# Kernel optimization log

Measured on AMD Instinct MI355X. Metric: run time of the kernel, lower is better.

Reference implementation:

```python
import jax, jax.numpy as jnp
import numpy as np

TEMP = 1.0  # temperature

def setup_inputs() -> dict:
    key = jax.random.key(0)
    ks = jax.random.split(key, 16)
    B, Cin, Cout, H, W, K, kk, A = 32, 64, 64, 128, 128, 4, 3, 16
    c_ = Cin + Cout
    r = lambda k, s: jax.random.normal(k, s, dtype=jnp.float32)
    return {
        'x': r(ks[0], (B, Cin, H, W)),
        'fc_w': r(ks[1], (A, Cin)) * 0.1,
        'ch_w': r(ks[2], (Cin, A)) * 0.1,
        'ch_b': jnp.zeros((Cin,), jnp.float32),
        'f_w': r(ks[3], (Cout, A)) * 0.1,
        'f_b': jnp.zeros((Cout,), jnp.float32),
        'sp_w': r(ks[4], (kk * kk, A)) * 0.1,
        'sp_b': jnp.zeros((kk * kk,), jnp.float32),
        'k_w': r(ks[5], (K, A)) * 0.1,
        'k_b': jnp.zeros((K,), jnp.float32),
        'fus_w1': r(ks[6], (c_ // 16, c_)) * 0.1,
        'fus_b1': jnp.zeros((c_ // 16,), jnp.float32),
        'fus_w2': r(ks[7], (c_, c_ // 16)) * 0.1,
        'fus_b2': jnp.zeros((c_,), jnp.float32),
        'weight': r(ks[8], (K, Cout, Cin, kk, kk)) * (1.0 / np.sqrt(Cin * kk * kk)),
    }

def reference(x, fc_w, ch_w, ch_b, f_w, f_b, sp_w, sp_b, k_w, k_b,
              fus_w1, fus_b1, fus_w2, fus_b2, weight):
    B, Cin, H, W = x.shape
    K, Cout, _, kk, _ = weight.shape
    # --- Attention branches (on globally pooled features) ---
    pooled = x.mean(axis=(2, 3))                      # (B, Cin)
    a = jax.nn.relu(pooled @ fc_w.T)                  # (B, A)
    ch_att = jax.nn.sigmoid(a @ ch_w.T + ch_b)        # (B, Cin)
    f_att = jax.nn.sigmoid(a @ f_w.T + f_b)           # (B, Cout)
    sp_att = jax.nn.sigmoid(a @ sp_w.T + sp_b).reshape(B, 1, 1, 1, kk, kk)
    k_att = jax.nn.softmax((a @ k_w.T + k_b) / TEMP, axis=1).reshape(B, K, 1, 1, 1, 1)
    # --- Attention fusion ---
    att = jnp.concatenate([ch_att, f_att], axis=1)    # (B, Cin+Cout)
    att2 = jax.nn.sigmoid(jax.nn.relu(att @ fus_w1.T + fus_b1) @ fus_w2.T + fus_b2)
    s1 = att2[:, :Cin].sum(axis=1)
    s2 = att2[:, Cin:].sum(axis=1)
    score = jax.nn.softmax(jnp.stack([s1, s2], axis=1) / TEMP, axis=1)
    w1 = score[:, 0][:, None, None, None]
    w2 = score[:, 1][:, None, None, None]
    # --- Apply channel attention, aggregate per-sample weights ---
    xm = w1 * x * ch_att[:, :, None, None]
    # (B,K,1,1,kk,kk)*(B,K,1,1,1,1)*(1,K,Cout,Cin,kk,kk) summed over K
    agg_w = (sp_att * k_att * weight[None]).sum(axis=1)  # (B, Cout, Cin, kk, kk)
    # --- Per-sample conv2d (stride 1, padding 1) ---
    def conv_one(xb, wb):
        return jax.lax.conv_general_dilated(
            xb[None], wb, window_strides=(1, 1), padding=[(1, 1), (1, 1)],
            dimension_numbers=('NCHW', 'OIHW', 'NCHW'))[0]
    out = jax.vmap(conv_one)(xm, agg_w)               # (B, Cout, H, W)
    return w2 * out * f_att[:, :, None, None]
```

## Files before the change

### kernel.cpp

```cpp
#include <hip/hip_runtime.h>
#include <math.h>
#include <stdint.h>

typedef short bf16x8 __attribute__((ext_vector_type(8)));
typedef float f32x16 __attribute__((ext_vector_type(16)));

#define WS_POOLED 0
#define WS_CIN    2048
#define WS_COUT   4096
#define WS_SP9    6144
#define WS_K4     6432
#define WS_WF     8192

static __device__ __forceinline__ unsigned f2bf(float f) {
  unsigned u = __builtin_bit_cast(unsigned, f);
  return (u + 0x7FFFu + ((u >> 16) & 1u)) >> 16;
}

__global__ __launch_bounds__(256) void pool_kernel(const float* __restrict__ x,
                                                   float* __restrict__ pooled) {
  const int bc = blockIdx.x;
  const int tid = threadIdx.x;
  const float4* p = (const float4*)(x + (size_t)bc * 16384);
  float s = 0.f;
  for (int j = tid; j < 4096; j += 256) {
    float4 v = p[j];
    s += (v.x + v.y) + (v.z + v.w);
  }
#pragma unroll
  for (int off = 32; off > 0; off >>= 1) s += __shfl_down(s, off, 64);
  __shared__ float red[4];
  if ((tid & 63) == 0) red[tid >> 6] = s;
  __syncthreads();
  if (tid == 0) pooled[bc] = (red[0] + red[1] + red[2] + red[3]) * (1.f / 16384.f);
}

__global__ __launch_bounds__(128) void att_kernel(
    const float* __restrict__ fc_w, const float* __restrict__ ch_w, const float* __restrict__ ch_b,
    const float* __restrict__ f_w,  const float* __restrict__ f_b,
    const float* __restrict__ sp_w, const float* __restrict__ sp_b,
    const float* __restrict__ k_w,  const float* __restrict__ k_b,
    const float* __restrict__ fus_w1, const float* __restrict__ fus_b1,
    const float* __restrict__ fus_w2, const float* __restrict__ fus_b2,
    float* __restrict__ ws) {
  const int b = blockIdx.x;
  const int t = threadIdx.x;
  __shared__ float s_pool[64], s_a[16], s_att[128], s_sp[9], s_k[4], s_h[8],
      s_att2[128], s_red[2], s_w12[2];

  if (t < 64) s_pool[t] = ws[WS_POOLED + b * 64 + t];
  __syncthreads();

  if (t < 16) {
    float s = 0.f;
    for (int c = 0; c < 64; ++c) s += s_pool[c] * fc_w[t * 64 + c];
    s_a[t] = fmaxf(s, 0.f);
  }
  __syncthreads();

  if (t < 64) {
    float s = ch_b[t];
    for (int j = 0; j < 16; ++j) s += s_a[j] * ch_w[t * 16 + j];
    s_att[t] = 1.f / (1.f + expf(-s));
  } else {
    const int o = t - 64;
    float s = f_b[o];
    for (int j = 0; j < 16; ++j) s += s_a[j] * f_w[o * 16 + j];
    s_att[t] = 1.f / (1.f + expf(-s));
  }
  if (t < 9) {
    float s = sp_b[t];
    for (int j = 0; j < 16; ++j) s += s_a[j] * sp_w[t * 16 + j];
    s_sp[t] = 1.f / (1.f + expf(-s));
  }
  if (t < 4) {
    float s = k_b[t];
    for (int j = 0; j < 16; ++j) s += s_a[j] * k_w[t * 16 + j];
    s_k[t] = s;
  }
  __syncthreads();

  if (t < 8) {
    float s = fus_b1[t];
    for (int c = 0; c < 128; ++c) s += s_att[c] * fus_w1[t * 128 + c];
    s_h[t] = fmaxf(s, 0.f);
  }
  if (t == 127) {
    float m = fmaxf(fmaxf(s_k[0], s_k[1]), fmaxf(s_k[2], s_k[3]));
    float e0 = expf(s_k[0] - m), e1 = expf(s_k[1] - m);
    float e2 = expf(s_k[2] - m), e3 = expf(s_k[3] - m);
    float inv = 1.f / (e0 + e1 + e2 + e3);
    s_k[0] = e0 * inv; s_k[1] = e1 * inv; s_k[2] = e2 * inv; s_k[3] = e3 * inv;
  }
  __syncthreads();

  {
    float s = fus_b2[t];
    for (int j = 0; j < 8; ++j) s += s_h[j] * fus_w2[t * 8 + j];
    s_att2[t] = 1.f / (1.f + expf(-s));
  }
  __syncthreads();

  if (t < 2) {
    float s = 0.f;
    for (int c = 0; c < 64; ++c) s += s_att2[t * 64 + c];
    s_red[t] = s;
  }
  __syncthreads();
  if (t == 0) {
    float m = fmaxf(s_red[0], s_red[1]);
    float e1 = expf(s_red[0] - m), e2 = expf(s_red[1] - m);
    float inv = 1.f / (e1 + e2);
    s_w12[0] = e1 * inv;
    s_w12[1] = e2 * inv;
  }
  __syncthreads();

  if (t < 64) {
    ws[WS_CIN  + b * 64 + t] = s_w12[0] * s_att[t];
    ws[WS_COUT + b * 64 + t] = s_w12[1] * s_att[64 + t];
  }
  if (t < 9) ws[WS_SP9 + b * 9 + t] = s_sp[t];
  if (t < 4) ws[WS_K4 + b * 4 + t] = s_k[t];
}

__global__ __launch_bounds__(256) void wf_kernel(const float* __restrict__ weight,
                                                 const float* __restrict__ ws,
                                                 unsigned short* __restrict__ wfb) {
  const int bo = blockIdx.x;
  const int b = bo >> 6, o = bo & 63;
  const float co = ws[WS_COUT + b * 64 + o];
  const float k0 = ws[WS_K4 + b * 4 + 0], k1 = ws[WS_K4 + b * 4 + 1];
  const float k2 = ws[WS_K4 + b * 4 + 2], k3 = ws[WS_K4 + b * 4 + 3];
  for (int idx = threadIdx.x; idx < 576; idx += 256) {
    const int pq = idx >> 6, i = idx & 63;
    const size_t wi = ((size_t)o * 64 + i) * 9 + pq;
    float s = k0 * weight[wi] + k1 * weight[36864 + wi] +
              k2 * weight[73728 + wi] + k3 * weight[110592 + wi];
    float v = co * ws[WS_SP9 + b * 9 + pq] * ws[WS_CIN + b * 64 + i] * s;
    wfb[((size_t)(b * 9 + pq) * 64 + o) * 64 + i] = (unsigned short)f2bf(v);
  }
}

__global__ __launch_bounds__(512, 2) void conv_kernel(const float* __restrict__ x,
                                                      const unsigned short* __restrict__ wfb,
                                                      float* __restrict__ out) {
  const int b  = blockIdx.x >> 5;
  const int h0 = (blockIdx.x & 31) << 2;
  const int tid = threadIdx.x;
  const int lane = tid & 63;
  const int wid = tid >> 6;
  const int rw = wid >> 1;
  const int obase = (wid & 1) << 5;
  const int l31 = lane & 31;
  const int hi = lane >> 5;

  __shared__ __align__(16) short sx[6 * 132 * 16];
  __shared__ __align__(16) short swf[576 * 16];

  f32x16 acc[4];
#pragma unroll
  for (int nt = 0; nt < 4; ++nt)
#pragma unroll
    for (int r = 0; r < 16; ++r) acc[nt][r] = 0.f;

  for (int ch = 0; ch < 4; ++ch) {
    const int c0 = ch << 4;
    __syncthreads();
    for (int idx = tid; idx < 1584; idx += 512) {
      const int c = idx % 132;
      const int t = idx / 132;
      const int r = t % 6;
      const int h8 = t / 6;
      const int gr = h0 - 1 + r, gc = c - 1;
      uint4 v = make_uint4(0u, 0u, 0u, 0u);
      if ((unsigned)gr < 128u && (unsigned)gc < 128u) {
        const float* xp = x + (((size_t)(b * 64 + c0 + h8 * 8) * 128 + gr) * 128 + gc);
        v.x = f2bf(xp[0])          | (f2bf(xp[16384])     << 16);
        v.y = f2bf(xp[2 * 16384])  | (f2bf(xp[3 * 16384]) << 16);
        v.z = f2bf(xp[4 * 16384])  | (f2bf(xp[5 * 16384]) << 16);
        v.w = f2bf(xp[6 * 16384])  | (f2bf(xp[7 * 16384]) << 16);
      }
      const int pix = r * 132 + c;
      const int byteoff = (pix * 32 + h8 * 16) ^ ((pix & 4) << 2);
      *(uint4*)((char*)sx + byteoff) = v;
    }
    for (int idx = tid; idx < 1152; idx += 512) {
      const int row = idx >> 1, h8 = idx & 1;
      uint4 v = *(const uint4*)(wfb + (((size_t)b * 576 + row) * 64 + c0 + h8 * 8));
      const int byteoff = (row * 32 + h8 * 16) ^ ((row & 4) << 2);
      *(uint4*)((char*)swf + byteoff) = v;
    }
    __syncthreads();

#pragma unroll
    for (int p = 0; p < 3; ++p) {
#pragma unroll
      for (int q = 0; q < 3; ++q) {
        const int arow = (p * 3 + q) * 64 + obase + l31;
        const int abyte = (arow * 32 + hi * 16) ^ ((arow & 4) << 2);
        bf16x8 af = *(const bf16x8*)((const char*)swf + abyte);
#pragma unroll
        for (int nt = 0; nt < 4; ++nt) {
          const int pix = (rw + p) * 132 + nt * 32 + q + l31;
          const int bbyte = (pix * 32 + hi * 16) ^ ((pix & 4) << 2);
          bf16x8 bf = *(const bf16x8*)((const char*)sx + bbyte);
          acc[nt] = __builtin_amdgcn_mfma_f32_32x32x16_bf16(af, bf, acc[nt], 0, 0, 0);
        }
      }
    }
  }

  const int h = h0 + rw;
#pragma unroll
  for (int nt = 0; nt < 4; ++nt) {
    const int col = nt * 32 + l31;
#pragma unroll
    for (int reg = 0; reg < 16; ++reg) {
      const int o = obase + (reg & 3) + ((reg >> 2) << 3) + (hi << 2);
      out[(((size_t)(b * 64 + o)) * 128 + h) * 128 + col] = acc[nt][reg];
    }
  }
}

extern "C" void kernel_launch(void* const* d_in, const int* in_sizes, int n_in,
                              void* d_out, int out_size, void* d_ws, size_t ws_size,
                              hipStream_t stream) {
  const float* x      = (const float*)d_in[0];
  const float* fc_w   = (const float*)d_in[1];
  const float* ch_w   = (const float*)d_in[2];
  const float* ch_b   = (const float*)d_in[3];
  const float* f_w    = (const float*)d_in[4];
  const float* f_b    = (const float*)d_in[5];
  const float* sp_w   = (const float*)d_in[6];
  const float* sp_b   = (const float*)d_in[7];
  const float* k_w    = (const float*)d_in[8];
  const float* k_b    = (const float*)d_in[9];
  const float* fus_w1 = (const float*)d_in[10];
  const float* fus_b1 = (const float*)d_in[11];
  const float* fus_w2 = (const float*)d_in[12];
  const float* fus_b2 = (const float*)d_in[13];
  const float* weight = (const float*)d_in[14];
  float* ws  = (float*)d_ws;
  float* out = (float*)d_out;
  unsigned short* wfb = (unsigned short*)(ws + WS_WF);

  pool_kernel<<<2048, 256, 0, stream>>>(x, ws + WS_POOLED);
  att_kernel<<<32, 128, 0, stream>>>(fc_w, ch_w, ch_b, f_w, f_b, sp_w, sp_b,
                                     k_w, k_b, fus_w1, fus_b1, fus_w2, fus_b2, ws);
  wf_kernel<<<2048, 256, 0, stream>>>(weight, ws, wfb);
  conv_kernel<<<1024, 512, 0, stream>>>(x, wfb, out);
}
```

Before: 137.3 us.

## Fuse pooling with bf16 NHWC conversion of x and feed conv from bf16

Adds a convert kernel that reads x once, writes a channel-last bf16 copy and per-block partial sums for pooling. This replaces the separate pool pass. The conv kernel then loads bf16 channel-contiguous tiles straight into shared memory, with lower register use so four blocks can share a CU, instead of converting fp32 NCHW inside the conv. It needs a workspace of about 67 MB and falls back to the old path when the workspace is smaller; the bf16 write and re-read add traffic of their own.

```diff
diff --git a/kernel.cpp b/kernel.cpp
--- a/kernel.cpp
+++ b/kernel.cpp
@@ -4,6 +4,7 @@
 
 typedef short bf16x8 __attribute__((ext_vector_type(8)));
 typedef float f32x16 __attribute__((ext_vector_type(16)));
+typedef unsigned short ushort_t;
 
 #define WS_POOLED 0
 #define WS_CIN    2048
@@ -12,9 +13,57 @@
 #define WS_K4     6432
 #define WS_WF     8192
 
+#define NP_CIN  65536
+#define NP_COUT 67584
+#define NP_SP9  69632
+#define NP_K4   69920
+#define NP_WFB_BYTES (512 * 1024)
+#define NP_XB_BYTES  (3 * 1024 * 1024)
+#define NP_NEED ((size_t)(3 * 1024 * 1024) + (size_t)(64 * 1024 * 1024))
+
 static __device__ __forceinline__ unsigned f2bf(float f) {
   unsigned u = __builtin_bit_cast(unsigned, f);
   return (u + 0x7FFFu + ((u >> 16) & 1u)) >> 16;
+}
+
+__global__ __launch_bounds__(256) void convert_kernel(const float* __restrict__ x,
+                                                      ushort_t* __restrict__ xb,
+                                                      float* __restrict__ part) {
+  const int b = blockIdx.x >> 5;
+  const int g = blockIdx.x & 31;
+  const int p0 = g << 9;
+  const int t = threadIdx.x;
+  const int w = t >> 6;
+  const int lane = t & 63;
+  __shared__ float s_part[4 * 64];
+
+  const int pa = p0 + 2 * t;
+  ushort_t* outp = xb + (size_t)(b * 16384 + pa) * 64;
+
+#pragma unroll 1
+  for (int g8 = 0; g8 < 8; ++g8) {
+    uint4 ca, cb;
+    unsigned* cap = (unsigned*)&ca;
+    unsigned* cbp = (unsigned*)&cb;
+#pragma unroll
+    for (int j = 0; j < 8; ++j) {
+      const int ci = g8 * 8 + j;
+      float2 v = *(const float2*)(x + ((size_t)(b * 64 + ci) * 16384) + pa);
+      float psum = v.x + v.y;
+#pragma unroll
+      for (int off = 32; off > 0; off >>= 1) psum += __shfl_down(psum, off, 64);
+      if (lane == 0) s_part[w * 64 + ci] = psum;
+      unsigned ba = f2bf(v.x), bb = f2bf(v.y);
+      if (j & 1) { cap[j >> 1] |= ba << 16; cbp[j >> 1] |= bb << 16; }
+      else       { cap[j >> 1]  = ba;       cbp[j >> 1]  = bb; }
+    }
+    *(uint4*)(outp + g8 * 8)      = ca;
+    *(uint4*)(outp + 64 + g8 * 8) = cb;
+  }
+  __syncthreads();
+  if (t < 64)
+    part[((size_t)b * 32 + g) * 64 + t] =
+        s_part[t] + s_part[64 + t] + s_part[128 + t] + s_part[192 + t];
 }
 
 __global__ __launch_bounds__(256) void pool_kernel(const float* __restrict__ x,
@@ -36,19 +85,29 @@
 }
 
 __global__ __launch_bounds__(128) void att_kernel(
+    const float* __restrict__ pin, int n_part,
     const float* __restrict__ fc_w, const float* __restrict__ ch_w, const float* __restrict__ ch_b,
     const float* __restrict__ f_w,  const float* __restrict__ f_b,
     const float* __restrict__ sp_w, const float* __restrict__ sp_b,
     const float* __restrict__ k_w,  const float* __restrict__ k_b,
     const float* __restrict__ fus_w1, const float* __restrict__ fus_b1,
     const float* __restrict__ fus_w2, const float* __restrict__ fus_b2,
-    float* __restrict__ ws) {
+    float* __restrict__ o_cin, float* __restrict__ o_cout,
+    float* __restrict__ o_sp9, float* __restrict__ o_k4) {
   const int b = blockIdx.x;
   const int t = threadIdx.x;
   __shared__ float s_pool[64], s_a[16], s_att[128], s_sp[9], s_k[4], s_h[8],
       s_att2[128], s_red[2], s_w12[2];
 
-  if (t < 64) s_pool[t] = ws[WS_POOLED + b * 64 + t];
+  if (t < 64) {
+    if (n_part > 0) {
+      float s = 0.f;
+      for (int g = 0; g < n_part; ++g) s += pin[((size_t)b * n_part + g) * 64 + t];
+      s_pool[t] = s * (1.f / 16384.f);
+    } else {
+      s_pool[t] = pin[b * 64 + t];
+    }
+  }
   __syncthreads();
 
   if (t < 16) {
@@ -117,34 +176,106 @@
   __syncthreads();
 
   if (t < 64) {
-    ws[WS_CIN  + b * 64 + t] = s_w12[0] * s_att[t];
-    ws[WS_COUT + b * 64 + t] = s_w12[1] * s_att[64 + t];
-  }
-  if (t < 9) ws[WS_SP9 + b * 9 + t] = s_sp[t];
-  if (t < 4) ws[WS_K4 + b * 4 + t] = s_k[t];
+    o_cin[b * 64 + t]  = s_w12[0] * s_att[t];
+    o_cout[b * 64 + t] = s_w12[1] * s_att[64 + t];
+  }
+  if (t < 9) o_sp9[b * 9 + t] = s_sp[t];
+  if (t < 4) o_k4[b * 4 + t] = s_k[t];
 }
 
 __global__ __launch_bounds__(256) void wf_kernel(const float* __restrict__ weight,
-                                                 const float* __restrict__ ws,
-                                                 unsigned short* __restrict__ wfb) {
+                                                 const float* __restrict__ cin,
+                                                 const float* __restrict__ cout_,
+                                                 const float* __restrict__ sp9,
+                                                 const float* __restrict__ k4,
+                                                 ushort_t* __restrict__ wfb) {
   const int bo = blockIdx.x;
   const int b = bo >> 6, o = bo & 63;
-  const float co = ws[WS_COUT + b * 64 + o];
-  const float k0 = ws[WS_K4 + b * 4 + 0], k1 = ws[WS_K4 + b * 4 + 1];
-  const float k2 = ws[WS_K4 + b * 4 + 2], k3 = ws[WS_K4 + b * 4 + 3];
+  const float co = cout_[b * 64 + o];
+  const float k0 = k4[b * 4 + 0], k1 = k4[b * 4 + 1];
+  const float k2 = k4[b * 4 + 2], k3 = k4[b * 4 + 3];
   for (int idx = threadIdx.x; idx < 576; idx += 256) {
     const int pq = idx >> 6, i = idx & 63;
     const size_t wi = ((size_t)o * 64 + i) * 9 + pq;
     float s = k0 * weight[wi] + k1 * weight[36864 + wi] +
               k2 * weight[73728 + wi] + k3 * weight[110592 + wi];
-    float v = co * ws[WS_SP9 + b * 9 + pq] * ws[WS_CIN + b * 64 + i] * s;
-    wfb[((size_t)(b * 9 + pq) * 64 + o) * 64 + i] = (unsigned short)f2bf(v);
-  }
-}
-
-__global__ __launch_bounds__(512, 2) void conv_kernel(const float* __restrict__ x,
-                                                      const unsigned short* __restrict__ wfb,
-                                                      float* __restrict__ out) {
+    float v = co * sp9[b * 9 + pq] * cin[b * 64 + i] * s;
+    wfb[((size_t)(b * 9 + pq) * 64 + o) * 64 + i] = (ushort_t)f2bf(v);
+  }
+}
+
+__global__ __launch_bounds__(512, 4) void conv_bf16(const ushort_t* __restrict__ xb,
+                                                    const ushort_t* __restrict__ wfb,
+                                                    float* __restrict__ out) {
+  const int b  = blockIdx.x >> 5;
+  const int h0 = (blockIdx.x & 31) << 2;
+  const int tid = threadIdx.x;
+  const int lane = tid & 63;
+  const int wid = tid >> 6;
+  const int rw = wid >> 1;
+  const int obase = (wid & 1) << 5;
+  const int l31 = lane & 31;
+  const int hi = lane >> 5;
+
+  __shared__ __align__(16) short sx[792 * 16];
+
+  f32x16 acc[4];
+#pragma unroll
+  for (int nt = 0; nt < 4; ++nt)
+#pragma unroll
+    for (int r = 0; r < 16; ++r) acc[nt][r] = 0.f;
+
+  const ushort_t* wfb_b = wfb + (size_t)b * 9 * 64 * 64;
+  const ushort_t* xb_b  = xb + (size_t)b * 16384 * 64;
+
+  for (int ch = 0; ch < 4; ++ch) {
+    const int c0 = ch << 4;
+    __syncthreads();
+    for (int s = tid; s < 1584; s += 512) {
+      const int pix = s >> 1, hseg = s & 1;
+      const int r = pix / 132;
+      const int c = pix - r * 132;
+      const int gr = h0 - 1 + r, gc = c - 1;
+      uint4 v = make_uint4(0u, 0u, 0u, 0u);
+      if ((unsigned)gr < 128u && (unsigned)gc < 128u)
+        v = *(const uint4*)(xb_b + (size_t)(gr * 128 + gc) * 64 + c0 + hseg * 8);
+      *(uint4*)((char*)sx + s * 16) = v;
+    }
+    bf16x8 af[9];
+#pragma unroll
+    for (int tap = 0; tap < 9; ++tap)
+      af[tap] = *(const bf16x8*)(wfb_b + ((tap * 64 + obase + l31) * 64) + c0 + hi * 8);
+    __syncthreads();
+
+#pragma unroll
+    for (int p = 0; p < 3; ++p) {
+#pragma unroll
+      for (int q = 0; q < 3; ++q) {
+#pragma unroll
+        for (int nt = 0; nt < 4; ++nt) {
+          const int pix = (rw + p) * 132 + nt * 32 + q + l31;
+          bf16x8 bf = *(const bf16x8*)((const char*)sx + pix * 32 + hi * 16);
+          acc[nt] = __builtin_amdgcn_mfma_f32_32x32x16_bf16(af[p * 3 + q], bf, acc[nt], 0, 0, 0);
+        }
+      }
+    }
+  }
+
+  const int h = h0 + rw;
+#pragma unroll
+  for (int nt = 0; nt < 4; ++nt) {
+    const int col = nt * 32 + l31;
+#pragma unroll
+    for (int reg = 0; reg < 16; ++reg) {
+      const int o = obase + (reg & 3) + ((reg >> 2) << 3) + (hi << 2);
+      out[(((size_t)(b * 64 + o)) * 128 + h) * 128 + col] = acc[nt][reg];
+    }
+  }
+}
+
+__global__ __launch_bounds__(512, 2) void conv_fp32(const float* __restrict__ x,
+                                                    const ushort_t* __restrict__ wfb,
+                                                    float* __restrict__ out) {
   const int b  = blockIdx.x >> 5;
   const int h0 = (blockIdx.x & 31) << 2;
   const int tid = threadIdx.x;
@@ -243,11 +374,31 @@
   const float* weight = (const float*)d_in[14];
   float* ws  = (float*)d_ws;
   float* out = (float*)d_out;
-  unsigned short* wfb = (unsigned short*)(ws + WS_WF);
-
-  pool_kernel<<<2048, 256, 0, stream>>>(x, ws + WS_POOLED);
-  att_kernel<<<32, 128, 0, stream>>>(fc_w, ch_w, ch_b, f_w, f_b, sp_w, sp_b,
-                                     k_w, k_b, fus_w1, fus_b1, fus_w2, fus_b2, ws);
-  wf_kernel<<<2048, 256, 0, stream>>>(weight, ws, wfb);
-  conv_kernel<<<1024, 512, 0, stream>>>(x, wfb, out);
-}
+
+  if (ws_size >= NP_NEED) {
+    float* part  = ws;
+    float* cin   = ws + NP_CIN;
+    float* cout_ = ws + NP_COUT;
+    float* sp9   = ws + NP_SP9;
+    float* k4    = ws + NP_K4;
+    ushort_t* wfb = (ushort_t*)((char*)d_ws + NP_WFB_BYTES);
+    ushort_t* xb  = (ushort_t*)((char*)d_ws + NP_XB_BYTES);
+
+    convert_kernel<<<1024, 256, 0, stream>>>(x, xb, part);
+    att_kernel<<<32, 128, 0, stream>>>(part, 32, fc_w, ch_w, ch_b, f_w, f_b,
+                                       sp_w, sp_b, k_w, k_b, fus_w1, fus_b1,
+                                       fus_w2, fus_b2, cin, cout_, sp9, k4);
+    wf_kernel<<<2048, 256, 0, stream>>>(weight, cin, cout_, sp9, k4, wfb);
+    conv_bf16<<<1024, 512, 0, stream>>>(xb, wfb, out);
+  } else {
+    ushort_t* wfb = (ushort_t*)(ws + WS_WF);
+    pool_kernel<<<2048, 256, 0, stream>>>(x, ws + WS_POOLED);
+    att_kernel<<<32, 128, 0, stream>>>(ws + WS_POOLED, 0, fc_w, ch_w, ch_b, f_w, f_b,
+                                       sp_w, sp_b, k_w, k_b, fus_w1, fus_b1,
+                                       fus_w2, fus_b2, ws + WS_CIN, ws + WS_COUT,
+                                       ws + WS_SP9, ws + WS_K4);
+    wf_kernel<<<2048, 256, 0, stream>>>(weight, ws + WS_CIN, ws + WS_COUT,
+                                        ws + WS_SP9, ws + WS_K4, wfb);
+    conv_fp32<<<1024, 512, 0, stream>>>(x, wfb, out);
+  }
+}
```

Result: slower. 277.4 us (+102.0%).

## Vectorize conv input staging, read weights from global, raise occupancy

Applied to the files above, without the earlier changes.

The conv kernel now stages the input tile with float4 loads: each of 408 threads loads 4 consecutive pixels across 8 channels, converts them to bf16 and writes them into a wider 136-column padded, XOR-swizzled LDS tile. The weight tile is no longer staged in LDS. MFMA A-fragments are read straight from global memory, which roughly halves LDS use and lets launch bounds rise to 4 blocks per CU. The aim is to cut scalar strided global loads and LDS traffic and to raise occupancy. The cost is repeated global/L2 reads of weights inside the MFMA loop and possible register pressure under the tighter bound. The attention and weight-fusion kernels are only refactored to take separate pointers.

```diff
diff --git a/kernel.cpp b/kernel.cpp
--- a/kernel.cpp
+++ b/kernel.cpp
@@ -4,6 +4,7 @@
 
 typedef short bf16x8 __attribute__((ext_vector_type(8)));
 typedef float f32x16 __attribute__((ext_vector_type(16)));
+typedef unsigned short ushort_t;
 
 #define WS_POOLED 0
 #define WS_CIN    2048
@@ -36,19 +37,21 @@
 }
 
 __global__ __launch_bounds__(128) void att_kernel(
+    const float* __restrict__ pooled,
     const float* __restrict__ fc_w, const float* __restrict__ ch_w, const float* __restrict__ ch_b,
     const float* __restrict__ f_w,  const float* __restrict__ f_b,
     const float* __restrict__ sp_w, const float* __restrict__ sp_b,
     const float* __restrict__ k_w,  const float* __restrict__ k_b,
     const float* __restrict__ fus_w1, const float* __restrict__ fus_b1,
     const float* __restrict__ fus_w2, const float* __restrict__ fus_b2,
-    float* __restrict__ ws) {
+    float* __restrict__ o_cin, float* __restrict__ o_cout,
+    float* __restrict__ o_sp9, float* __restrict__ o_k4) {
   const int b = blockIdx.x;
   const int t = threadIdx.x;
   __shared__ float s_pool[64], s_a[16], s_att[128], s_sp[9], s_k[4], s_h[8],
       s_att2[128], s_red[2], s_w12[2];
 
-  if (t < 64) s_pool[t] = ws[WS_POOLED + b * 64 + t];
+  if (t < 64) s_pool[t] = pooled[b * 64 + t];
   __syncthreads();
 
   if (t < 16) {
@@ -117,33 +120,36 @@
   __syncthreads();
 
   if (t < 64) {
-    ws[WS_CIN  + b * 64 + t] = s_w12[0] * s_att[t];
-    ws[WS_COUT + b * 64 + t] = s_w12[1] * s_att[64 + t];
-  }
-  if (t < 9) ws[WS_SP9 + b * 9 + t] = s_sp[t];
-  if (t < 4) ws[WS_K4 + b * 4 + t] = s_k[t];
+    o_cin[b * 64 + t]  = s_w12[0] * s_att[t];
+    o_cout[b * 64 + t] = s_w12[1] * s_att[64 + t];
+  }
+  if (t < 9) o_sp9[b * 9 + t] = s_sp[t];
+  if (t < 4) o_k4[b * 4 + t] = s_k[t];
 }
 
 __global__ __launch_bounds__(256) void wf_kernel(const float* __restrict__ weight,
-                                                 const float* __restrict__ ws,
-                                                 unsigned short* __restrict__ wfb) {
+                                                 const float* __restrict__ cin,
+                                                 const float* __restrict__ cout_,
+                                                 const float* __restrict__ sp9,
+                                                 const float* __restrict__ k4,
+                                                 ushort_t* __restrict__ wfb) {
   const int bo = blockIdx.x;
   const int b = bo >> 6, o = bo & 63;
-  const float co = ws[WS_COUT + b * 64 + o];
-  const float k0 = ws[WS_K4 + b * 4 + 0], k1 = ws[WS_K4 + b * 4 + 1];
-  const float k2 = ws[WS_K4 + b * 4 + 2], k3 = ws[WS_K4 + b * 4 + 3];
+  const float co = cout_[b * 64 + o];
+  const float k0 = k4[b * 4 + 0], k1 = k4[b * 4 + 1];
+  const float k2 = k4[b * 4 + 2], k3 = k4[b * 4 + 3];
   for (int idx = threadIdx.x; idx < 576; idx += 256) {
     const int pq = idx >> 6, i = idx & 63;
     const size_t wi = ((size_t)o * 64 + i) * 9 + pq;
     float s = k0 * weight[wi] + k1 * weight[36864 + wi] +
               k2 * weight[73728 + wi] + k3 * weight[110592 + wi];
-    float v = co * ws[WS_SP9 + b * 9 + pq] * ws[WS_CIN + b * 64 + i] * s;
-    wfb[((size_t)(b * 9 + pq) * 64 + o) * 64 + i] = (unsigned short)f2bf(v);
-  }
-}
-
-__global__ __launch_bounds__(512, 2) void conv_kernel(const float* __restrict__ x,
-                                                      const unsigned short* __restrict__ wfb,
+    float v = co * sp9[b * 9 + pq] * cin[b * 64 + i] * s;
+    wfb[((size_t)(b * 9 + pq) * 64 + o) * 64 + i] = (ushort_t)f2bf(v);
+  }
+}
+
+__global__ __launch_bounds__(512, 4) void conv_kernel(const float* __restrict__ x,
+                                                      const ushort_t* __restrict__ wfb,
                                                       float* __restrict__ out) {
   const int b  = blockIdx.x >> 5;
   const int h0 = (blockIdx.x & 31) << 2;
@@ -155,8 +161,7 @@
   const int l31 = lane & 31;
   const int hi = lane >> 5;
 
-  __shared__ __align__(16) short sx[6 * 132 * 16];
-  __shared__ __align__(16) short swf[576 * 16];
+  __shared__ __align__(16) short sx[816 * 16];
 
   f32x16 acc[4];
 #pragma unroll
@@ -164,32 +169,40 @@
 #pragma unroll
     for (int r = 0; r < 16; ++r) acc[nt][r] = 0.f;
 
+  const ushort_t* wfb_b = wfb + (size_t)b * 9 * 64 * 64;
+
+  const bool sactive = tid < 408;
+  int so = 0, sr = 0, sc = 0;
+  if (sactive) { so = tid / 204; const int rem = tid % 204; sr = rem / 34; sc = rem % 34; }
+  const int gr  = h0 - 1 + sr;
+  const int gcb = sc * 4 - 4;
+  const bool inb = sactive && ((unsigned)gr < 128u) && ((unsigned)gcb < 128u);
+  const int pixb = sr * 136 + sc * 4;
+  const int key = ((pixb >> 2) & 7) << 4;
+  const float* xrow = x + ((size_t)(b * 64) * 16384) + gr * 128 + gcb;
+
   for (int ch = 0; ch < 4; ++ch) {
-    const int c0 = ch << 4;
     __syncthreads();
-    for (int idx = tid; idx < 1584; idx += 512) {
-      const int c = idx % 132;
-      const int t = idx / 132;
-      const int r = t % 6;
-      const int h8 = t / 6;
-      const int gr = h0 - 1 + r, gc = c - 1;
-      uint4 v = make_uint4(0u, 0u, 0u, 0u);
-      if ((unsigned)gr < 128u && (unsigned)gc < 128u) {
-        const float* xp = x + (((size_t)(b * 64 + c0 + h8 * 8) * 128 + gr) * 128 + gc);
-        v.x = f2bf(xp[0])          | (f2bf(xp[16384])     << 16);
-        v.y = f2bf(xp[2 * 16384])  | (f2bf(xp[3 * 16384]) << 16);
-        v.z = f2bf(xp[4 * 16384])  | (f2bf(xp[5 * 16384]) << 16);
-        v.w = f2bf(xp[6 * 16384])  | (f2bf(xp[7 * 16384]) << 16);
+    if (inb) {
+      const int c0 = ch * 16 + so * 8;
+      float4 v[8];
+#pragma unroll
+      for (int j = 0; j < 8; ++j)
+        v[j] = *(const float4*)(xrow + (size_t)(c0 + j) * 16384);
+#pragma unroll
+      for (int j = 0; j < 4; ++j) {
+        uint4 u;
+        u.x = f2bf(((const float*)&v[0])[j]) | (f2bf(((const float*)&v[1])[j]) << 16);
+        u.y = f2bf(((const float*)&v[2])[j]) | (f2bf(((const float*)&v[3])[j]) << 16);
+        u.z = f2bf(((const float*)&v[4])[j]) | (f2bf(((const float*)&v[5])[j]) << 16);
+        u.w = f2bf(((const float*)&v[6])[j]) | (f2bf(((const float*)&v[7])[j]) << 16);
+        *(uint4*)((char*)sx + ((((pixb + j) * 32) + so * 16) ^ key)) = u;
       }
-      const int pix = r * 132 + c;
-      const int byteoff = (pix * 32 + h8 * 16) ^ ((pix & 4) << 2);
-      *(uint4*)((char*)sx + byteoff) = v;
-    }
-    for (int idx = tid; idx < 1152; idx += 512) {
-      const int row = idx >> 1, h8 = idx & 1;
-      uint4 v = *(const uint4*)(wfb + (((size_t)b * 576 + row) * 64 + c0 + h8 * 8));
-      const int byteoff = (row * 32 + h8 * 16) ^ ((row & 4) << 2);
-      *(uint4*)((char*)swf + byteoff) = v;
+    } else if (sactive) {
+      const uint4 z = make_uint4(0u, 0u, 0u, 0u);
+#pragma unroll
+      for (int j = 0; j < 4; ++j)
+        *(uint4*)((char*)sx + ((((pixb + j) * 32) + so * 16) ^ key)) = z;
     }
     __syncthreads();
 
@@ -197,14 +210,13 @@
     for (int p = 0; p < 3; ++p) {
 #pragma unroll
       for (int q = 0; q < 3; ++q) {
-        const int arow = (p * 3 + q) * 64 + obase + l31;
-        const int abyte = (arow * 32 + hi * 16) ^ ((arow & 4) << 2);
-        bf16x8 af = *(const bf16x8*)((const char*)swf + abyte);
+        const int tap = p * 3 + q;
+        bf16x8 af = *(const bf16x8*)(wfb_b + ((tap * 64 + obase + l31) * 64) + ch * 16 + hi * 8);
 #pragma unroll
         for (int nt = 0; nt < 4; ++nt) {
-          const int pix = (rw + p) * 132 + nt * 32 + q + l31;
-          const int bbyte = (pix * 32 + hi * 16) ^ ((pix & 4) << 2);
-          bf16x8 bf = *(const bf16x8*)((const char*)sx + bbyte);
+          const int pix = (rw + p) * 136 + 3 + q + nt * 32 + l31;
+          const int boff = ((pix * 32) + hi * 16) ^ (((pix >> 2) & 7) << 4);
+          bf16x8 bf = *(const bf16x8*)((const char*)sx + boff);
           acc[nt] = __builtin_amdgcn_mfma_f32_32x32x16_bf16(af, bf, acc[nt], 0, 0, 0);
         }
       }
@@ -243,11 +255,14 @@
   const float* weight = (const float*)d_in[14];
   float* ws  = (float*)d_ws;
   float* out = (float*)d_out;
-  unsigned short* wfb = (unsigned short*)(ws + WS_WF);
+  ushort_t* wfb = (ushort_t*)(ws + WS_WF);
 
   pool_kernel<<<2048, 256, 0, stream>>>(x, ws + WS_POOLED);
-  att_kernel<<<32, 128, 0, stream>>>(fc_w, ch_w, ch_b, f_w, f_b, sp_w, sp_b,
-                                     k_w, k_b, fus_w1, fus_b1, fus_w2, fus_b2, ws);
-  wf_kernel<<<2048, 256, 0, stream>>>(weight, ws, wfb);
+  att_kernel<<<32, 128, 0, stream>>>(ws + WS_POOLED, fc_w, ch_w, ch_b, f_w, f_b,
+                                     sp_w, sp_b, k_w, k_b, fus_w1, fus_b1,
+                                     fus_w2, fus_b2, ws + WS_CIN, ws + WS_COUT,
+                                     ws + WS_SP9, ws + WS_K4);
+  wf_kernel<<<2048, 256, 0, stream>>>(weight, ws + WS_CIN, ws + WS_COUT,
+                                      ws + WS_SP9, ws + WS_K4, wfb);
   conv_kernel<<<1024, 512, 0, stream>>>(x, wfb, out);
 }
```

Measured after the change: 146.1 us. 1.06x slower.
